# Kernel tuning notes

Hardware: AMD Instinct MI355X
Metric: run time of the kernel (lower is better)

The kernel has to match this reference:

```python
import jax, jax.numpy as jnp
import numpy as np

B, S, D, H = 4, 2048, 1024, 16
HD = D // H
EPS = 1e-5


def gelu_tanh(x):
    c = jnp.sqrt(jnp.asarray(2.0 / jnp.pi, x.dtype))
    return x * 0.5 * (1.0 + jnp.tanh(c * (x + 0.044715 * x ** 3)))


def layer_norm(x, scale, shift):
    mean = jnp.mean(x, axis=-1, keepdims=True)
    var = jnp.var(x, axis=-1, keepdims=True)  # unbiased=False
    return scale * ((x - mean) / jnp.sqrt(var + EPS)) + shift


def setup_inputs() -> dict:
    key = jax.random.key(0)
    ks = jax.random.split(key, 8)
    s = 0.02
    return {
        "x": jax.random.normal(ks[0], (B, S, D), jnp.float32),
        "Wqkv": jax.random.normal(ks[1], (D, 3 * D), jnp.float32) * s,
        "Wout": jax.random.normal(ks[2], (D, D), jnp.float32) * s,
        "bout": jnp.zeros((D,), jnp.float32),
        "W1": jax.random.normal(ks[3], (D, 4 * D), jnp.float32) * s,
        "b1": jnp.zeros((4 * D,), jnp.float32),
        "W2": jax.random.normal(ks[4], (4 * D, D), jnp.float32) * s,
        "b2": jnp.zeros((D,), jnp.float32),
        "g1": jnp.ones((D,), jnp.float32),
        "s1": jnp.zeros((D,), jnp.float32),
        "g2": jnp.ones((D,), jnp.float32),
        "s2": jnp.zeros((D,), jnp.float32),
    }


def reference(x, Wqkv, Wout, bout, W1, b1, W2, b2, g1, s1, g2, s2):
    # --- attention branch ---
    h = layer_norm(x, g1, s1)
    qkv = h @ Wqkv  # [B,S,3D]
    qkv = qkv.reshape(B, S, 3, H, HD).transpose(2, 0, 3, 1, 4)  # [3,B,H,S,hd]
    q, k, v = qkv[0], qkv[1], qkv[2]
    scores = jnp.einsum("bhqd,bhkd->bhqk", q, k)
    causal = jnp.triu(jnp.ones((S, S), bool), k=1)
    scores = jnp.where(causal, -jnp.inf, scores)
    attn = jax.nn.softmax(scores / jnp.sqrt(jnp.asarray(HD, x.dtype)), axis=-1)
    ctx = jnp.einsum("bhqk,bhkd->bhqd", attn, v)
    ctx = ctx.transpose(0, 2, 1, 3).reshape(B, S, D)
    x = x + (ctx @ Wout + bout)
    # --- MLP branch ---
    h = layer_norm(x, g2, s2)
    h = gelu_tanh(h @ W1 + b1) @ W2 + b2
    return x + h
```

## Files before the change

kernel.cpp:

```cpp
#include <hip/hip_runtime.h>
#include <stdint.h>

typedef unsigned short u16;
typedef unsigned long long u64;
typedef __attribute__((ext_vector_type(8))) short bf16x8;
typedef __attribute__((ext_vector_type(4))) float f32x4;

#define DEV __device__ __forceinline__

DEV u16 f2bf(float f) {
  union { float f; unsigned u; } v; v.f = f;
  unsigned r = (v.u + 0x7fffu + ((v.u >> 16) & 1u)) >> 16;
  return (u16)r;
}

#define GLDS(g, l) __builtin_amdgcn_global_load_lds( \
    (const __attribute__((address_space(1))) void*)(g), \
    (__attribute__((address_space(3))) void*)(l), 16, 0, 0)

#define BAR() __builtin_amdgcn_s_barrier()
#define LGKM0() asm volatile("s_waitcnt lgkmcnt(0)" ::: "memory")
#define VMW(n) asm volatile("s_waitcnt vmcnt(" #n ")" ::: "memory")
#define SCHED0() __builtin_amdgcn_sched_barrier(0)

__global__ __launch_bounds__(256) void k_transpose_all(
    const float* __restrict__ Wqkv, const float* __restrict__ Wout,
    const float* __restrict__ W1, const float* __restrict__ W2,
    u16* __restrict__ WqkvT, u16* __restrict__ WoutT,
    u16* __restrict__ W1T, u16* __restrict__ W2T) {
  int id = blockIdx.x;
  const float* in; u16* out; int K, N, nx, base;
  if (id < 3072)      { in = Wqkv; out = WqkvT; K = 1024; N = 3072; nx = 96;  base = 0; }
  else if (id < 4096) { in = Wout; out = WoutT; K = 1024; N = 1024; nx = 32;  base = 3072; }
  else if (id < 8192) { in = W1;   out = W1T;   K = 1024; N = 4096; nx = 128; base = 4096; }
  else                { in = W2;   out = W2T;   K = 4096; N = 1024; nx = 32;  base = 8192; }
  int seg = id - base, bx = seg % nx, by = seg / nx;
  __shared__ float tile[32][33];
  int tx = threadIdx.x & 31, ty = threadIdx.x >> 5;
#pragma unroll
  for (int r = 0; r < 32; r += 8)
    tile[ty + r][tx] = in[(size_t)(by * 32 + ty + r) * N + bx * 32 + tx];
  __syncthreads();
#pragma unroll
  for (int r = 0; r < 32; r += 8)
    out[(size_t)(bx * 32 + ty + r) * K + by * 32 + tx] = f2bf(tile[tx][ty + r]);
}

__global__ __launch_bounds__(256) void k_layernorm(
    const float* __restrict__ x, const float* __restrict__ gamma,
    const float* __restrict__ beta, u16* __restrict__ out) {
  int row = blockIdx.x, t = threadIdx.x;
  const float4 v = ((const float4*)(x + (size_t)row * 1024))[t];
  float sum = v.x + v.y + v.z + v.w;
  float sq = v.x * v.x + v.y * v.y + v.z * v.z + v.w * v.w;
#pragma unroll
  for (int o = 32; o >= 1; o >>= 1) {
    sum += __shfl_down(sum, o);
    sq += __shfl_down(sq, o);
  }
  __shared__ float red[8];
  if ((t & 63) == 0) { red[(t >> 6) * 2] = sum; red[(t >> 6) * 2 + 1] = sq; }
  __syncthreads();
  sum = red[0] + red[2] + red[4] + red[6];
  sq = red[1] + red[3] + red[5] + red[7];
  float mean = sum * (1.0f / 1024.0f);
  float var = sq * (1.0f / 1024.0f) - mean * mean;
  float rstd = rsqrtf(var + 1e-5f);
  float4 g = ((const float4*)gamma)[t];
  float4 b = ((const float4*)beta)[t];
  ushort4 o4;
  o4.x = f2bf(g.x * (v.x - mean) * rstd + b.x);
  o4.y = f2bf(g.y * (v.y - mean) * rstd + b.y);
  o4.z = f2bf(g.z * (v.z - mean) * rstd + b.z);
  o4.w = f2bf(g.w * (v.w - mean) * rstd + b.w);
  ((ushort4*)(out + (size_t)row * 1024))[t] = o4;
}

struct EpiQKV {
  u16 *Q, *K2, *VT;
  DEV void operator()(int r, int c0, const f32x4& v) const {
    int three = c0 >> 10, h = (c0 >> 6) & 15, hd = c0 & 63;
    int b = r >> 11, s = r & 2047;
    int bh = b * 16 + h;
    ushort4 o;
    o.x = f2bf(v[0]); o.y = f2bf(v[1]); o.z = f2bf(v[2]); o.w = f2bf(v[3]);
    if (three == 0)
      *(ushort4*)&Q[((size_t)bh * 2048 + s) * 64 + hd] = o;
    else if (three == 1)
      *(ushort4*)&K2[((size_t)bh * 2048 + s) * 64 + hd] = o;
    else {
      VT[((size_t)bh * 64 + hd + 0) * 2048 + s] = o.x;
      VT[((size_t)bh * 64 + hd + 1) * 2048 + s] = o.y;
      VT[((size_t)bh * 64 + hd + 2) * 2048 + s] = o.z;
      VT[((size_t)bh * 64 + hd + 3) * 2048 + s] = o.w;
    }
  }
};

struct EpiBiasResid {
  const float* bias; const float* resid; float* out; int N;
  DEV void operator()(int r, int c0, const f32x4& v) const {
    size_t idx = (size_t)r * N + c0;
    float4 bb = *(const float4*)&bias[c0];
    float4 rr = *(const float4*)&resid[idx];
    float4 o;
    o.x = v[0] + bb.x + rr.x; o.y = v[1] + bb.y + rr.y;
    o.z = v[2] + bb.z + rr.z; o.w = v[3] + bb.w + rr.w;
    *(float4*)&out[idx] = o;
  }
};

struct EpiBiasGelu {
  const float* bias; u16* out; int N;
  DEV float gelu(float xx) const {
    float u = 0.7978845608f * (xx + 0.044715f * xx * xx * xx);
    float e = __expf(2.0f * u);
    float th = 1.0f - 2.0f / (e + 1.0f);
    return 0.5f * xx * (1.0f + th);
  }
  DEV void operator()(int r, int c0, const f32x4& v) const {
    float4 bb = *(const float4*)&bias[c0];
    ushort4 o;
    o.x = f2bf(gelu(v[0] + bb.x)); o.y = f2bf(gelu(v[1] + bb.y));
    o.z = f2bf(gelu(v[2] + bb.z)); o.w = f2bf(gelu(v[3] + bb.w));
    *(ushort4*)&out[(size_t)r * N + c0] = o;
  }
};

#define STG8(tk, d) do { \
    GLDS(gA + (tk) * 64,                        &As[d][0][t * 8]); \
    GLDS(gA + (tk) * 64 + (size_t)64 * K,       &As[d][0][t * 8 + 2048]); \
    GLDS(gA + (tk) * 64 + 32,                   &As[d][1][t * 8]); \
    GLDS(gA + (tk) * 64 + 32 + (size_t)64 * K,  &As[d][1][t * 8 + 2048]); \
    GLDS(gB + (tk) * 64,                        &Bs[d][0][t * 8]); \
    GLDS(gB + (tk) * 64 + (size_t)64 * K,       &Bs[d][0][t * 8 + 2048]); \
    GLDS(gB + (tk) * 64 + 32,                   &Bs[d][1][t * 8]); \
    GLDS(gB + (tk) * 64 + 32 + (size_t)64 * K,  &Bs[d][1][t * 8 + 2048]); \
  } while (0)

template <typename Epi>
__global__ __launch_bounds__(256) void k_gemm_tn(
    const u16* __restrict__ A, const u16* __restrict__ Bt, int K, Epi epi) {
  __shared__ u16 As[2][2][128 * 32];
  __shared__ u16 Bs[2][2][128 * 32];
  const int t = threadIdx.x;
  const int bm = blockIdx.x, bn = blockIdx.y;
  const int lane = t & 63, w = t >> 6;
  const int wm = w >> 1, wn = w & 1;
  const int quad = lane >> 4, l16 = lane & 15;
  f32x4 acc[4][4] = {};
  const u16* gA = A + (size_t)(bm * 128 + (t >> 2)) * K + (t & 3) * 8;
  const u16* gB = Bt + (size_t)(bn * 128 + (t >> 2)) * K + (t & 3) * 8;
  const int NT = K >> 6;

  STG8(0, 0);
  STG8(1, 1);
  VMW(8);
  BAR();

  for (int T = 0; T < NT; ++T) {
    const int d = T & 1;
#pragma unroll
    for (int kk = 0; kk < 2; ++kk) {
      bf16x8 af[4], bfr[4];
#pragma unroll
      for (int mt = 0; mt < 4; ++mt)
        af[mt] = *(const bf16x8*)&As[d][kk][(wm * 64 + mt * 16 + l16) * 32 + quad * 8];
#pragma unroll
      for (int nt = 0; nt < 4; ++nt)
        bfr[nt] = *(const bf16x8*)&Bs[d][kk][(wn * 64 + nt * 16 + l16) * 32 + quad * 8];
#pragma unroll
      for (int mt = 0; mt < 4; ++mt)
#pragma unroll
        for (int nt = 0; nt < 4; ++nt)
          acc[mt][nt] = __builtin_amdgcn_mfma_f32_16x16x32_bf16(
              bfr[nt], af[mt], acc[mt][nt], 0, 0, 0);
    }
    SCHED0();
    BAR();
    SCHED0();
    if (T + 2 < NT) {
      STG8(T + 2, d);
      VMW(8);
    } else {
      VMW(0);
    }
    BAR();
  }

  const int r0 = bm * 128 + wm * 64 + l16;
  const int c0 = bn * 128 + wn * 64 + quad * 4;
#pragma unroll
  for (int mt = 0; mt < 4; ++mt)
#pragma unroll
    for (int nt = 0; nt < 4; ++nt)
      epi(r0 + mt * 16, c0 + nt * 16, acc[mt][nt]);
}

#define PW 72

#define ATT_LOAD(kr, vr, k0_) do { \
  _Pragma("unroll") for (int j = 0; j < 4; ++j) { \
    int ch = t + 256 * j, r = ch >> 4, cc = (ch & 15) * 4; \
    kr[j] = *(const u64*)(Kbase + (size_t)((k0_) + r) * 64 + cc); \
    vr[j] = *(const u64*)(Vbase + (size_t)r * 2048 + (k0_) + cc); \
  } } while (0)

#define ATT_WRITE(kr, vr) do { \
  _Pragma("unroll") for (int j = 0; j < 4; ++j) { \
    int ch = t + 256 * j, r = ch >> 4, cc = (ch & 15) * 4; \
    *(u64*)&Ks[r * PW + cc] = kr[j]; \
    *(u64*)&Vs[r * PW + cc] = vr[j]; \
  } } while (0)

__global__ __launch_bounds__(256) void k_attn(
    const u16* __restrict__ Qg, const u16* __restrict__ Kg,
    const u16* __restrict__ VTg, u16* __restrict__ ctx) {
  const int bh = blockIdx.x;
  const int qt = 31 - blockIdx.y;
  const int b = bh >> 4, h = bh & 15;
  const int t = threadIdx.x, lane = t & 63, w = t >> 6;
  const int quad = lane >> 4, l16 = lane & 15;
  const int q0 = qt * 64;
  __shared__ u16 Qs[64 * PW], Ks[64 * PW], Vs[64 * PW];
  __shared__ u16 Ps[4][16 * PW];
  __shared__ float l_lds[4][16];
  const u16* Qbase = Qg + (size_t)bh * (2048 * 64);
  const u16* Kbase = Kg + (size_t)bh * (2048 * 64);
  const u16* Vbase = VTg + (size_t)bh * (64 * 2048);
#pragma unroll
  for (int j = 0; j < 4; ++j) {
    int ch = t + 256 * j, r = ch >> 4, cc = (ch & 15) * 4;
    *(u64*)&Qs[r * PW + cc] = *(const u64*)(Qbase + (size_t)(q0 + r) * 64 + cc);
  }
  __syncthreads();
  bf16x8 qf0 = *(const bf16x8*)&Qs[(w * 16 + l16) * PW + quad * 8];
  bf16x8 qf1 = *(const bf16x8*)&Qs[(w * 16 + l16) * PW + 32 + quad * 8];
  const int qrow = q0 + w * 16 + l16;
  const float c1 = 0.18033688011f;
  float lsum = 0.f;
  f32x4 acco[4] = {};

  auto tile = [&](int kt) {
    const int k0 = kt * 64;
    f32x4 sacc[4] = {};
#pragma unroll
    for (int kk = 0; kk < 2; ++kk) {
      bf16x8 qf = kk ? qf1 : qf0;
#pragma unroll
      for (int nt = 0; nt < 4; ++nt) {
        bf16x8 kf = *(const bf16x8*)&Ks[(nt * 16 + l16) * PW + kk * 32 + quad * 8];
        sacc[nt] = __builtin_amdgcn_mfma_f32_16x16x32_bf16(kf, qf, sacc[nt], 0, 0, 0);
      }
    }
    const bool diag = (kt == qt);
    float ls = 0.f;
#pragma unroll
    for (int nt = 0; nt < 4; ++nt) {
      ushort4 o;
#pragma unroll
      for (int reg = 0; reg < 4; ++reg) {
        float p = __builtin_amdgcn_exp2f(sacc[nt][reg] * c1);
        if (diag && (k0 + nt * 16 + quad * 4 + reg > qrow)) p = 0.f;
        ls += p;
        (&o.x)[reg] = f2bf(p);
      }
      *(ushort4*)&Ps[w][l16 * PW + nt * 16 + quad * 4] = o;
    }
    ls += __shfl_xor(ls, 16);
    ls += __shfl_xor(ls, 32);
    lsum += ls;
#pragma unroll
    for (int kk = 0; kk < 2; ++kk) {
      bf16x8 pf = *(const bf16x8*)&Ps[w][l16 * PW + kk * 32 + quad * 8];
#pragma unroll
      for (int nt = 0; nt < 4; ++nt) {
        bf16x8 vf = *(const bf16x8*)&Vs[(nt * 16 + l16) * PW + kk * 32 + quad * 8];
        acco[nt] = __builtin_amdgcn_mfma_f32_16x16x32_bf16(pf, vf, acco[nt], 0, 0, 0);
      }
    }
  };

  u64 kra[4], vra[4], krb[4], vrb[4];
  ATT_LOAD(kra, vra, 0);
  int kt = 0;
  while (true) {
    VMW(0);
    BAR();
    ATT_WRITE(kra, vra);
    if (kt + 1 <= qt) ATT_LOAD(krb, vrb, (kt + 1) * 64);
    LGKM0();
    BAR();
    tile(kt);
    if (++kt > qt) break;
    VMW(0);
    BAR();
    ATT_WRITE(krb, vrb);
    if (kt + 1 <= qt) ATT_LOAD(kra, vra, (kt + 1) * 64);
    LGKM0();
    BAR();
    tile(kt);
    if (++kt > qt) break;
  }

  if (quad == 0) l_lds[w][l16] = lsum;
  float4 lv = *(const float4*)&l_lds[w][quad * 4];
  float inv[4];
  inv[0] = 1.0f / lv.x; inv[1] = 1.0f / lv.y;
  inv[2] = 1.0f / lv.z; inv[3] = 1.0f / lv.w;
#pragma unroll
  for (int nt = 0; nt < 4; ++nt)
#pragma unroll
    for (int reg = 0; reg < 4; ++reg) {
      float o = acco[nt][reg] * inv[reg];
      int q = q0 + w * 16 + quad * 4 + reg;
      ctx[((size_t)(b * 2048 + q)) * 1024 + h * 64 + nt * 16 + l16] = f2bf(o);
    }
}

extern "C" void kernel_launch(void* const* d_in, const int* in_sizes, int n_in,
                              void* d_out, int out_size, void* d_ws, size_t ws_size,
                              hipStream_t stream) {
  (void)in_sizes; (void)n_in; (void)out_size; (void)ws_size;
  const float* x    = (const float*)d_in[0];
  const float* Wqkv = (const float*)d_in[1];
  const float* Wout = (const float*)d_in[2];
  const float* bout = (const float*)d_in[3];
  const float* W1   = (const float*)d_in[4];
  const float* b1   = (const float*)d_in[5];
  const float* W2   = (const float*)d_in[6];
  const float* b2   = (const float*)d_in[7];
  const float* g1   = (const float*)d_in[8];
  const float* s1   = (const float*)d_in[9];
  const float* g2   = (const float*)d_in[10];
  const float* s2   = (const float*)d_in[11];

  char* ws = (char*)d_ws;
  u16*   WqkvT = (u16*)(ws + 0);
  u16*   WoutT = (u16*)(ws + 6291456);
  u16*   W1T   = (u16*)(ws + 8388608);
  u16*   W2T   = (u16*)(ws + 16777216);
  float* x1    = (float*)(ws + 25165824);
  u16*   h12   = (u16*)(ws + 58720256);
  u16*   Qb    = (u16*)(ws + 75497472);
  u16*   Kb    = (u16*)(ws + 92274688);
  u16*   VTb   = (u16*)(ws + 109051904);
  u16*   ctx   = (u16*)(ws + 125829120);
  u16*   a1    = (u16*)(ws + 75497472);

  k_transpose_all<<<12288, 256, 0, stream>>>(Wqkv, Wout, W1, W2,
                                             WqkvT, WoutT, W1T, W2T);

  k_layernorm<<<8192, 256, 0, stream>>>(x, g1, s1, h12);
  k_gemm_tn<<<dim3(64, 24), 256, 0, stream>>>(h12, WqkvT, 1024,
                                              EpiQKV{Qb, Kb, VTb});
  k_attn<<<dim3(64, 32), 256, 0, stream>>>(Qb, Kb, VTb, ctx);
  k_gemm_tn<<<dim3(64, 8), 256, 0, stream>>>(ctx, WoutT, 1024,
                                             EpiBiasResid{bout, x, x1, 1024});
  k_layernorm<<<8192, 256, 0, stream>>>(x1, g2, s2, h12);
  k_gemm_tn<<<dim3(64, 32), 256, 0, stream>>>(h12, W1T, 1024,
                                              EpiBiasGelu{b1, a1, 4096});
  k_gemm_tn<<<dim3(64, 8), 256, 0, stream>>>(a1, W2T, 4096,
                                             EpiBiasResid{b2, x1, (float*)d_out, 1024});
}
```

Measured before the change: 519.8 us.

## Add 256x256-tile 512-thread GEMM for QKV and FFN-up projections

Adds a GEMM kernel with 256x256 output tiles and 8 waves, each computing 128x64, and uses it for the QKV and W1 projections. Larger tiles raise arithmetic intensity and cut global/LDS traffic per FLOP compared with the 128x128 kernel. In exchange each wave holds more accumulators, so register pressure rises. The grids also shrink to 384 and 512 blocks, which may leave CUs unevenly loaded (tail effects). Shared memory use is 128KB per block with launch_bounds(512,2), so occupancy may be limited.

Measured after the change: 530.1 us. About the same (+2.0%).

```diff
diff --git a/kernel.cpp b/kernel.cpp
--- a/kernel.cpp
+++ b/kernel.cpp
@@ -197,6 +197,76 @@
       epi(r0 + mt * 16, c0 + nt * 16, acc[mt][nt]);
 }
 
+#define STG8W(tk, d) do { \
+    GLDS(gA + (tk) * 64,                         &As[d][0][t * 8]); \
+    GLDS(gA + (tk) * 64 + (size_t)128 * K,       &As[d][0][t * 8 + 4096]); \
+    GLDS(gA + (tk) * 64 + 32,                    &As[d][1][t * 8]); \
+    GLDS(gA + (tk) * 64 + 32 + (size_t)128 * K,  &As[d][1][t * 8 + 4096]); \
+    GLDS(gB + (tk) * 64,                         &Bs[d][0][t * 8]); \
+    GLDS(gB + (tk) * 64 + (size_t)128 * K,       &Bs[d][0][t * 8 + 4096]); \
+    GLDS(gB + (tk) * 64 + 32,                    &Bs[d][1][t * 8]); \
+    GLDS(gB + (tk) * 64 + 32 + (size_t)128 * K,  &Bs[d][1][t * 8 + 4096]); \
+  } while (0)
+
+template <typename Epi>
+__global__ __launch_bounds__(512, 2) void k_gemm_wide(
+    const u16* __restrict__ A, const u16* __restrict__ Bt, int K, Epi epi) {
+  __shared__ u16 As[2][2][256 * 32];
+  __shared__ u16 Bs[2][2][256 * 32];
+  const int t = threadIdx.x;
+  const int bm = blockIdx.x, bn = blockIdx.y;
+  const int lane = t & 63, w = t >> 6;
+  const int wm = w >> 2, wn = w & 3;
+  const int quad = lane >> 4, l16 = lane & 15;
+  f32x4 acc[8][4] = {};
+  const u16* gA = A + (size_t)(bm * 256 + (t >> 2)) * K + (t & 3) * 8;
+  const u16* gB = Bt + (size_t)(bn * 256 + (t >> 2)) * K + (t & 3) * 8;
+  const int NT = K >> 6;
+
+  STG8W(0, 0);
+  STG8W(1, 1);
+  VMW(8);
+  BAR();
+
+  for (int T = 0; T < NT; ++T) {
+    const int d = T & 1;
+#pragma unroll
+    for (int kk = 0; kk < 2; ++kk) {
+      bf16x8 af[8], bfr[4];
+#pragma unroll
+      for (int mt = 0; mt < 8; ++mt)
+        af[mt] = *(const bf16x8*)&As[d][kk][(wm * 128 + mt * 16 + l16) * 32 + quad * 8];
+#pragma unroll
+      for (int nt = 0; nt < 4; ++nt)
+        bfr[nt] = *(const bf16x8*)&Bs[d][kk][(wn * 64 + nt * 16 + l16) * 32 + quad * 8];
+#pragma unroll
+      for (int mt = 0; mt < 8; ++mt)
+#pragma unroll
+        for (int nt = 0; nt < 4; ++nt)
+          acc[mt][nt] = __builtin_amdgcn_mfma_f32_16x16x32_bf16(
+              bfr[nt], af[mt], acc[mt][nt], 0, 0, 0);
+    }
+    SCHED0();
+    BAR();
+    SCHED0();
+    if (T + 2 < NT) {
+      STG8W(T + 2, d);
+      VMW(8);
+    } else {
+      VMW(0);
+    }
+    BAR();
+  }
+
+  const int r0 = bm * 256 + wm * 128 + l16;
+  const int c0 = bn * 256 + wn * 64 + quad * 4;
+#pragma unroll
+  for (int mt = 0; mt < 8; ++mt)
+#pragma unroll
+    for (int nt = 0; nt < 4; ++nt)
+      epi(r0 + mt * 16, c0 + nt * 16, acc[mt][nt]);
+}
+
 #define PW 72
 
 #define ATT_LOAD(kr, vr, k0_) do { \
@@ -352,14 +422,14 @@
                                              WqkvT, WoutT, W1T, W2T);
 
   k_layernorm<<<8192, 256, 0, stream>>>(x, g1, s1, h12);
-  k_gemm_tn<<<dim3(64, 24), 256, 0, stream>>>(h12, WqkvT, 1024,
-                                              EpiQKV{Qb, Kb, VTb});
+  k_gemm_wide<<<dim3(32, 12), 512, 0, stream>>>(h12, WqkvT, 1024,
+                                                EpiQKV{Qb, Kb, VTb});
   k_attn<<<dim3(64, 32), 256, 0, stream>>>(Qb, Kb, VTb, ctx);
   k_gemm_tn<<<dim3(64, 8), 256, 0, stream>>>(ctx, WoutT, 1024,
                                              EpiBiasResid{bout, x, x1, 1024});
   k_layernorm<<<8192, 256, 0, stream>>>(x1, g2, s2, h12);
-  k_gemm_tn<<<dim3(64, 32), 256, 0, stream>>>(h12, W1T, 1024,
-                                              EpiBiasGelu{b1, a1, 4096});
+  k_gemm_wide<<<dim3(32, 16), 512, 0, stream>>>(h12, W1T, 1024,
+                                                EpiBiasGelu{b1, a1, 4096});
   k_gemm_tn<<<dim3(64, 8), 256, 0, stream>>>(a1, W2T, 4096,
                                              EpiBiasResid{b2, x1, (float*)d_out, 1024});
 }
```
